# Kernel tuning notes

Measured on AMD Instinct MI355X. Metric: run time of the kernel, lower is better.

## Reference

```python
import jax, jax.numpy as jnp
import numpy as np

N_NODES = 10000


def gcn_conv(x, W, b, src, dst, num_nodes):
    """PyG GCNConv: add self-loops, symmetric deg^{-1/2} normalization,
    linear transform (no bias in lin), scatter-add aggregation, then bias."""
    xw = x @ W  # (N, H)
    # degree on A + I (self-loops added)
    deg = jnp.zeros((num_nodes,), dtype=x.dtype).at[dst].add(1.0) + 1.0
    dinv = jax.lax.rsqrt(deg)  # (N,)
    norm = dinv[src] * dinv[dst]  # (E,)
    msg = xw[src] * norm[:, None]  # (E, H) gathered messages
    agg = jax.ops.segment_sum(msg, dst, num_segments=num_nodes)
    # self-loop contribution: norm_ii = dinv_i^2
    agg = agg + xw * (dinv * dinv)[:, None]
    return agg + b


def setup_inputs() -> dict:
    key = jax.random.key(0)
    k1, k2, k3, k4 = jax.random.split(key, 4)
    N, F, H, E = N_NODES, 256, 512, 320000
    x = jax.random.normal(k1, (N, F), dtype=jnp.float32)
    edge_index = jax.random.randint(k2, (2, E), 0, N, dtype=jnp.int64)
    W1 = jax.random.normal(k3, (F, H), dtype=jnp.float32) * (1.0 / np.sqrt(F))
    b1 = jnp.zeros((H,), dtype=jnp.float32)
    W2 = jax.random.normal(k4, (H, F), dtype=jnp.float32) * (1.0 / np.sqrt(H))
    b2 = jnp.zeros((F,), dtype=jnp.float32)
    return {"x": x, "edge_index": edge_index, "W1": W1, "b1": b1, "W2": W2, "b2": b2}


def reference(x, edge_index, W1, b1, W2, b2):
    src, dst = edge_index[0], edge_index[1]
    h = jax.nn.relu(gcn_conv(x, W1, b1, src, dst, N_NODES))
    h = jax.nn.relu(gcn_conv(h, W2, b2, src, dst, N_NODES))
    # global_max_pool with single graph (batch all zeros) -> (1, F)
    return jnp.max(h, axis=0, keepdims=True)
```

## Files before the change

kernel.cpp:

```cpp
#include <hip/hip_runtime.h>

#define NNODES 10000
#define MP 10112
#define F 256
#define H 512
#define CAP 128
#define H1STR 520

typedef _Float16 half8 __attribute__((ext_vector_type(8)));
typedef float floatx4 __attribute__((ext_vector_type(4)));
typedef float floatx8 __attribute__((ext_vector_type(8)));

__global__ __launch_bounds__(256) void prep_k(const float* __restrict__ W1,
                                              const float* __restrict__ W2,
                                              const float* __restrict__ x,
                                              _Float16* __restrict__ W1t,
                                              _Float16* __restrict__ W2t,
                                              _Float16* __restrict__ xh,
                                              int* __restrict__ cnt) {
  int gt = blockIdx.x * 256 + threadIdx.x;
  if (gt < NNODES) cnt[gt] = 0;
  if (gt < H * F) {
    W1t[gt] = (_Float16)W1[(gt & 255) * H + (gt >> 8)];
    W2t[gt] = (_Float16)W2[(gt & 511) * F + (gt >> 9)];
  }
  if (gt < NNODES * F / 8) {
    floatx8 v = *(const floatx8*)(x + (size_t)gt * 8);
    *(half8*)(xh + (size_t)gt * 8) = __builtin_convertvector(v, half8);
  }
}

__global__ __launch_bounds__(256) void build_k(const int* __restrict__ src,
                                               const int* __restrict__ dst,
                                               int* __restrict__ cnt,
                                               int* __restrict__ csr, int E) {
  int e = blockIdx.x * blockDim.x + threadIdx.x;
  if (e < E) {
    int d = dst[e];
    int p = atomicAdd(&cnt[d], 1);
    if (p < CAP) csr[(size_t)d * CAP + p] = src[e];
  }
}

template <bool FUSE_MAX>
__global__ __launch_bounds__(256) void aggb_k(const _Float16* __restrict__ in,
                                              const int* __restrict__ cnt,
                                              const int* __restrict__ csr,
                                              const float* __restrict__ bias,
                                              _Float16* __restrict__ outh,
                                              float* __restrict__ out) {
  __shared__ float smem[2048];
  int tid = threadIdx.x;
  int lane = tid & 63, wvi = tid >> 6;
  int half = lane >> 5, hl = lane & 31;
  int f0 = hl * 8;
  int node = (blockIdx.x * 4 + wvi) * 2 + half;
  floatx8 bb = {};
  if (FUSE_MAX) bb = *(const floatx8*)(bias + f0);
  int deg = min(cnt[node], CAP);
  float di = rsqrtf((float)(deg + 1));
  const int* bucket = csr + (size_t)node * CAP;
  floatx8 acc = {};
  for (int c = 0; c < deg; c += 32) {
    int mm = min(32, deg - c);
    int sv = 0; float wvv = 0.f;
    if (hl < mm) {
      sv = bucket[c + hl];
      wvv = rsqrtf((float)(cnt[sv] + 1));
    }
    #pragma unroll
    for (int b = 0; b < 2; b++) {
      int base = b * 16;
      if (base < mm) {
        int sj[16]; float wj[16];
        #pragma unroll
        for (int u = 0; u < 16; u++) {
          int l = (half << 5) | (base + u);
          sj[u] = __shfl(sv, l, 64);
          wj[u] = __shfl(wvv, l, 64);
        }
        half8 hv[16];
        #pragma unroll
        for (int u = 0; u < 16; u++)
          hv[u] = *(const half8*)(in + (size_t)sj[u] * F + f0);
        #pragma unroll
        for (int u = 0; u < 16; u++)
          acc += wj[u] * __builtin_convertvector(hv[u], floatx8);
      }
    }
  }
  half8 xsv = *(const half8*)(in + (size_t)node * F + f0);
  floatx8 tot = di * acc + (di * di) * __builtin_convertvector(xsv, floatx8);
  if (FUSE_MAX) {
    tot += bb;
    floatx8 lmax;
    #pragma unroll
    for (int t = 0; t < 8; t++) lmax[t] = fmaxf(tot[t], 0.f);
    float* srow = smem + (size_t)(wvi * 2 + half) * 256;
    *(floatx8*)(srow + f0) = lmax;
    __syncthreads();
    float m = smem[tid];
    #pragma unroll
    for (int r = 1; r < 8; r++) m = fmaxf(m, smem[r * 256 + tid]);
    atomicMax((int*)&out[tid], __float_as_int(m));
  } else {
    *(half8*)(outh + (size_t)node * F + f0) = __builtin_convertvector(tot, half8);
  }
}

__global__ __launch_bounds__(256) void gemm12_k(const _Float16* __restrict__ A,
                                                const _Float16* __restrict__ W1t,
                                                const float* __restrict__ b1,
                                                const _Float16* __restrict__ W2t,
                                                _Float16* __restrict__ C) {
  __shared__ _Float16 h1[16 * H1STR];
  int lane = threadIdx.x & 63;
  int wv = threadIdx.x >> 6;
  int r = lane & 15, q = lane >> 4;
  int m0 = blockIdx.x * 16;

  {
    floatx4 acc[8] = {};
    const _Float16* Ap = A + (size_t)(m0 + r) * F + q * 8;
    const _Float16* Bp = W1t + (size_t)(wv * 128 + r) * F + q * 8;
    for (int k0 = 0; k0 < F; k0 += 32) {
      half8 a = *(const half8*)(Ap + k0);
      half8 b[8];
      #pragma unroll
      for (int j = 0; j < 8; j++) b[j] = *(const half8*)(Bp + (size_t)j * 16 * F + k0);
      #pragma unroll
      for (int j = 0; j < 8; j++)
        acc[j] = __builtin_amdgcn_mfma_f32_16x16x32_f16(a, b[j], acc[j], 0, 0, 0);
    }
    #pragma unroll
    for (int j = 0; j < 8; j++) {
      int n = wv * 128 + j * 16 + r;
      float bv = b1[n];
      #pragma unroll
      for (int rr = 0; rr < 4; rr++)
        h1[(q * 4 + rr) * H1STR + n] = (_Float16)fmaxf(acc[j][rr] + bv, 0.f);
    }
  }
  __syncthreads();

  {
    floatx4 acc[4] = {};
    const _Float16* Bp = W2t + (size_t)(wv * 64 + r) * H + q * 8;
    for (int k0 = 0; k0 < H; k0 += 32) {
      half8 a = *(const half8*)(h1 + r * H1STR + k0 + q * 8);
      half8 b[4];
      #pragma unroll
      for (int j = 0; j < 4; j++) b[j] = *(const half8*)(Bp + (size_t)j * 16 * H + k0);
      #pragma unroll
      for (int j = 0; j < 4; j++)
        acc[j] = __builtin_amdgcn_mfma_f32_16x16x32_f16(a, b[j], acc[j], 0, 0, 0);
    }
    #pragma unroll
    for (int j = 0; j < 4; j++) {
      int n = wv * 64 + j * 16 + r;
      #pragma unroll
      for (int rr = 0; rr < 4; rr++) {
        int row = m0 + q * 4 + rr;
        C[(size_t)row * F + n] = (_Float16)acc[j][rr];
      }
    }
  }
}

extern "C" void kernel_launch(void* const* d_in, const int* in_sizes, int n_in,
                              void* d_out, int out_size, void* d_ws, size_t ws_size,
                              hipStream_t stream) {
  const float* x  = (const float*)d_in[0];
  const int*   ei = (const int*)d_in[1];
  const float* W1 = (const float*)d_in[2];
  const float* b1 = (const float*)d_in[3];
  const float* W2 = (const float*)d_in[4];
  const float* b2 = (const float*)d_in[5];
  const int E = in_sizes[1] / 2;
  const int N = NNODES;
  const int* src = ei;
  const int* dst = ei + E;

  char* w = (char*)d_ws;
  size_t off = 0;
  auto take = [&](size_t bytes) -> void* {
    void* p = w + off;
    off += (bytes + 255) & ~(size_t)255;
    return p;
  };
  int*       cnt    = (int*)take((size_t)N * 4);
  int*       csr    = (int*)take((size_t)N * CAP * 4);
  _Float16*  W1t    = (_Float16*)take((size_t)H * F * 2);
  _Float16*  W2t    = (_Float16*)take((size_t)F * H * 2);
  _Float16*  xh     = (_Float16*)take((size_t)N * F * 2);
  _Float16*  axh    = (_Float16*)take((size_t)MP * F * 2);
  _Float16*  xw2h   = (_Float16*)take((size_t)MP * F * 2);

  prep_k<<<1250, 256, 0, stream>>>(W1, W2, x, W1t, W2t, xh, cnt);
  build_k<<<(E + 255) / 256, 256, 0, stream>>>(src, dst, cnt, csr, E);
  aggb_k<false><<<1250, 256, 0, stream>>>(xh, cnt, csr, nullptr, axh, nullptr);
  gemm12_k<<<MP / 16, 256, 0, stream>>>(axh, W1t, b1, W2t, xw2h);
  aggb_k<true><<<1250, 256, 0, stream>>>(xw2h, cnt, csr, b2, nullptr, (float*)d_out);
}
```

Measured before the change: 192.5 us.

## Split fused two-layer GEMM into separate column-tiled thin GEMM kernels

Replaces the fused GEMM kernel, which kept the 16-row hidden tile in shared memory between the two matmuls, with two launches of a templated thin GEMM. Each launch splits the output columns across grid.y, so each wave computes only 32 columns. The aim is more blocks in flight and fewer registers per wave than the 632-block fused kernel. In exchange the fp16 hidden activation (MP x 512) makes a round trip through global memory, and there is an extra launch.

```diff
diff --git a/kernel.cpp b/kernel.cpp
--- a/kernel.cpp
+++ b/kernel.cpp
@@ -5,7 +5,6 @@
 #define F 256
 #define H 512
 #define CAP 128
-#define H1STR 520
 
 typedef _Float16 half8 __attribute__((ext_vector_type(8)));
 typedef float floatx4 __attribute__((ext_vector_type(4)));
@@ -108,61 +107,36 @@
   }
 }
 
-__global__ __launch_bounds__(256) void gemm12_k(const _Float16* __restrict__ A,
-                                                const _Float16* __restrict__ W1t,
-                                                const float* __restrict__ b1,
-                                                const _Float16* __restrict__ W2t,
-                                                _Float16* __restrict__ C) {
-  __shared__ _Float16 h1[16 * H1STR];
+template <int K, int NT, bool RELU>
+__global__ __launch_bounds__(256) void gemmthin_k(const _Float16* __restrict__ A,
+                                                  const _Float16* __restrict__ Bt,
+                                                  const float* __restrict__ bias,
+                                                  _Float16* __restrict__ C) {
   int lane = threadIdx.x & 63;
   int wv = threadIdx.x >> 6;
   int r = lane & 15, q = lane >> 4;
   int m0 = blockIdx.x * 16;
-
-  {
-    floatx4 acc[8] = {};
-    const _Float16* Ap = A + (size_t)(m0 + r) * F + q * 8;
-    const _Float16* Bp = W1t + (size_t)(wv * 128 + r) * F + q * 8;
-    for (int k0 = 0; k0 < F; k0 += 32) {
-      half8 a = *(const half8*)(Ap + k0);
-      half8 b[8];
-      #pragma unroll
-      for (int j = 0; j < 8; j++) b[j] = *(const half8*)(Bp + (size_t)j * 16 * F + k0);
-      #pragma unroll
-      for (int j = 0; j < 8; j++)
-        acc[j] = __builtin_amdgcn_mfma_f32_16x16x32_f16(a, b[j], acc[j], 0, 0, 0);
-    }
+  int n0 = blockIdx.y * 128 + wv * 32;
+  floatx4 acc[2] = {};
+  const _Float16* Ap = A + (size_t)(m0 + r) * K + q * 8;
+  const _Float16* Bp = Bt + (size_t)(n0 + r) * K + q * 8;
+  for (int k0 = 0; k0 < K; k0 += 32) {
+    half8 a  = *(const half8*)(Ap + k0);
+    half8 b0 = *(const half8*)(Bp + k0);
+    half8 b1 = *(const half8*)(Bp + 16 * K + k0);
+    acc[0] = __builtin_amdgcn_mfma_f32_16x16x32_f16(a, b0, acc[0], 0, 0, 0);
+    acc[1] = __builtin_amdgcn_mfma_f32_16x16x32_f16(a, b1, acc[1], 0, 0, 0);
+  }
+  #pragma unroll
+  for (int j = 0; j < 2; j++) {
+    int n = n0 + j * 16 + r;
+    float bv = RELU ? bias[n] : 0.f;
     #pragma unroll
-    for (int j = 0; j < 8; j++) {
-      int n = wv * 128 + j * 16 + r;
-      float bv = b1[n];
-      #pragma unroll
-      for (int rr = 0; rr < 4; rr++)
-        h1[(q * 4 + rr) * H1STR + n] = (_Float16)fmaxf(acc[j][rr] + bv, 0.f);
-    }
-  }
-  __syncthreads();
-
-  {
-    floatx4 acc[4] = {};
-    const _Float16* Bp = W2t + (size_t)(wv * 64 + r) * H + q * 8;
-    for (int k0 = 0; k0 < H; k0 += 32) {
-      half8 a = *(const half8*)(h1 + r * H1STR + k0 + q * 8);
-      half8 b[4];
-      #pragma unroll
-      for (int j = 0; j < 4; j++) b[j] = *(const half8*)(Bp + (size_t)j * 16 * H + k0);
-      #pragma unroll
-      for (int j = 0; j < 4; j++)
-        acc[j] = __builtin_amdgcn_mfma_f32_16x16x32_f16(a, b[j], acc[j], 0, 0, 0);
-    }
-    #pragma unroll
-    for (int j = 0; j < 4; j++) {
-      int n = wv * 64 + j * 16 + r;
-      #pragma unroll
-      for (int rr = 0; rr < 4; rr++) {
-        int row = m0 + q * 4 + rr;
-        C[(size_t)row * F + n] = (_Float16)acc[j][rr];
-      }
+    for (int rr = 0; rr < 4; rr++) {
+      int row = m0 + q * 4 + rr;
+      float v = acc[j][rr] + bv;
+      if (RELU) v = fmaxf(v, 0.f);
+      C[(size_t)row * NT + n] = (_Float16)v;
     }
   }
 }
@@ -194,11 +168,13 @@
   _Float16*  W2t    = (_Float16*)take((size_t)F * H * 2);
   _Float16*  xh     = (_Float16*)take((size_t)N * F * 2);
   _Float16*  axh    = (_Float16*)take((size_t)MP * F * 2);
+  _Float16*  h1h    = (_Float16*)take((size_t)MP * H * 2);
   _Float16*  xw2h   = (_Float16*)take((size_t)MP * F * 2);
 
   prep_k<<<1250, 256, 0, stream>>>(W1, W2, x, W1t, W2t, xh, cnt);
   build_k<<<(E + 255) / 256, 256, 0, stream>>>(src, dst, cnt, csr, E);
   aggb_k<false><<<1250, 256, 0, stream>>>(xh, cnt, csr, nullptr, axh, nullptr);
-  gemm12_k<<<MP / 16, 256, 0, stream>>>(axh, W1t, b1, W2t, xw2h);
+  gemmthin_k<F, H, true><<<dim3(MP / 16, 4), 256, 0, stream>>>(axh, W1t, b1, h1h);
+  gemmthin_k<H, F, false><<<dim3(MP / 16, 2), 256, 0, stream>>>(h1h, W2t, nullptr, xw2h);
   aggb_k<true><<<1250, 256, 0, stream>>>(xw2h, cnt, csr, b2, nullptr, (float*)d_out);
 }
```

After: 201.8 us. 1.05x slower.
